# Optimization experiments

Hardware: AMD Instinct MI355X
Metric: run time of the kernel (lower is better)

Reference implementation:

```python
import jax, jax.numpy as jnp
import numpy as np

D_MODEL = 768
N_HEADS = 12
D_K = D_MODEL // N_HEADS
BATCH = 1
SEQ = 4096


def setup_inputs() -> dict:
    key = jax.random.key(0)
    kx, kq, kk, kv, ko = jax.random.split(key, 5)
    s = 1.0 / np.sqrt(D_MODEL)
    return {
        "x": jax.random.normal(kx, (BATCH, SEQ, D_MODEL), dtype=jnp.float32),
        "wq": jax.random.normal(kq, (D_MODEL, D_MODEL), dtype=jnp.float32) * s,
        "wk": jax.random.normal(kk, (D_MODEL, D_MODEL), dtype=jnp.float32) * s,
        "wv": jax.random.normal(kv, (D_MODEL, D_MODEL), dtype=jnp.float32) * s,
        "wo": jax.random.normal(ko, (D_MODEL, D_MODEL), dtype=jnp.float32) * s,
    }


def reference(x, wq, wk, wv, wo):
    B, S, D = x.shape
    H, dk = N_HEADS, D_K
    # nn.Linear(x) = x @ W.T ; reshape to [B,H,S,dk]
    def proj(w):
        return (x @ w.T).reshape(B, S, H, dk).transpose(0, 2, 1, 3)
    q, k, v = proj(wq), proj(wk), proj(wv)
    scores = jnp.einsum('bhqd,bhkd->bhqk', q, k) / np.sqrt(dk).astype(np.float32)
    attn = jax.nn.softmax(scores, axis=-1)
    out = jnp.einsum('bhqk,bhkd->bhqd', attn, v)
    out = out.transpose(0, 2, 1, 3).reshape(B, S, D)
    return out @ wo.T
```

## Files before the change

kernel.cpp:

```cpp
#include <hip/hip_runtime.h>
#include <stdint.h>

#define SEQ 4096
#define DMODEL 768
#define NHEADS 12
#define DKH 64

typedef __attribute__((ext_vector_type(8))) short short8;
typedef __attribute__((ext_vector_type(4))) float floatx4;
typedef __attribute__((ext_vector_type(16))) float floatx16;

__device__ __forceinline__ unsigned short f2bf(float f) {
    unsigned int u = __float_as_uint(f);
    u += 0x7fffu + ((u >> 16) & 1u);
    return (unsigned short)(u >> 16);
}

__device__ __forceinline__ float exp2fast(float x) {
    return __builtin_amdgcn_exp2f(x);
}

__device__ __forceinline__ unsigned int cvt_pk_bf16(float lo, float hi) {
    unsigned int r;
    asm("v_cvt_pk_bf16_f32 %0, %1, %2" : "=v"(r) : "v"(lo), "v"(hi));
    return r;
}

__device__ __forceinline__ int swz(int row, int colb) {
    return colb ^ ((row & 7) << 4);
}

__device__ __forceinline__ void async_copy16(void* lds, const void* g) {
    __builtin_amdgcn_global_load_lds(
        (const __attribute__((address_space(1))) void*)g,
        (__attribute__((address_space(3))) void*)lds,
        16, 0, 0);
}

__global__ __launch_bounds__(256) void castk(const float* __restrict__ src,
                                             unsigned short* __restrict__ dst,
                                             int n4) {
    int i = blockIdx.x * 256 + threadIdx.x;
    if (i >= n4) return;
    float4 v = ((const float4*)src)[i];
    ushort4 o;
    o.x = f2bf(v.x); o.y = f2bf(v.y); o.z = f2bf(v.z); o.w = f2bf(v.w);
    ((ushort4*)dst)[i] = o;
}

__global__ __launch_bounds__(256) void castw(const float* __restrict__ w0,
                                             const float* __restrict__ w1,
                                             const float* __restrict__ w2,
                                             const float* __restrict__ w3,
                                             unsigned short* __restrict__ dst) {
    int b = blockIdx.x;
    int wsel = b / 576;
    int i = (b % 576) * 256 + threadIdx.x;
    const float* src = (wsel == 0) ? w0 : (wsel == 1) ? w1 : (wsel == 2) ? w2 : w3;
    float4 v = ((const float4*)src)[i];
    ushort4 o;
    o.x = f2bf(v.x); o.y = f2bf(v.y); o.z = f2bf(v.z); o.w = f2bf(v.w);
    ((ushort4*)(dst + (size_t)wsel * 589824))[i] = o;
}

#define STAGE_G(bsel, kb)                                                              \
    do {                                                                               \
        char* As_ = smem + (bsel) * 24576;                                             \
        _Pragma("unroll") for (int ii = 0; ii < 4; ii++) {                             \
            int o = ii * 4096 + t * 16;                                                \
            int row = o >> 7, colb = o & 127;                                          \
            async_copy16(As_ + ii * 4096 + wid * 1024,                                 \
                         (const char*)A + ((size_t)(rowBase + row) * DMODEL + (kb)) * 2 \
                             + swz(row, colb));                                        \
        }                                                                              \
        _Pragma("unroll") for (int ii = 0; ii < 2; ii++) {                             \
            int o = ii * 4096 + t * 16;                                                \
            int row = o >> 7, colb = o & 127;                                          \
            async_copy16(As_ + 16384 + ii * 4096 + wid * 1024,                         \
                         (const char*)B + ((size_t)(colBase + row) * DMODEL + (kb)) * 2 \
                             + swz(row, colb));                                        \
        }                                                                              \
    } while (0)

#define GEMM_COMPUTE(As, Bs)                                                           \
    do {                                                                               \
        short8 a_[4][2], b_[2][2];                                                     \
        _Pragma("unroll") for (int m = 0; m < 4; m++)                                  \
            _Pragma("unroll") for (int kk = 0; kk < 2; kk++) {                         \
                int row = wr * 64 + m * 16 + lr;                                       \
                int colb = kk * 64 + lg * 16;                                          \
                a_[m][kk] = *(const short8*)((As) + row * 128 + swz(row, colb));       \
            }                                                                          \
        _Pragma("unroll") for (int n = 0; n < 2; n++)                                  \
            _Pragma("unroll") for (int kk = 0; kk < 2; kk++) {                         \
                int row = wc * 32 + n * 16 + lr;                                       \
                int colb = kk * 64 + lg * 16;                                          \
                b_[n][kk] = *(const short8*)((Bs) + row * 128 + swz(row, colb));       \
            }                                                                          \
        _Pragma("unroll") for (int m = 0; m < 4; m++)                                  \
            _Pragma("unroll") for (int n = 0; n < 2; n++)                              \
                _Pragma("unroll") for (int kk = 0; kk < 2; kk++)                       \
                    acc[m][n] = __builtin_amdgcn_mfma_f32_16x16x32_bf16(               \
                        a_[m][kk], b_[n][kk], acc[m][n], 0, 0, 0);                     \
    } while (0)

__global__ __launch_bounds__(256, 2)
void gemm_qkv(const unsigned short* __restrict__ A,
              const unsigned short* __restrict__ W,
              unsigned short* __restrict__ OutBase, float qscale) {
    __shared__ __align__(128) char smem[49152];

    const int t = threadIdx.x;
    const int wid = t >> 6, lane = t & 63;
    const int lr = lane & 15, lg = lane >> 4;
    const int wr = wid >> 1, wc = wid & 1;
    const int rowBase = blockIdx.x * 128;
    const int proj = blockIdx.y / 12;
    const int colBase = (blockIdx.y % 12) * 64;
    const unsigned short* B = W + (size_t)proj * 589824;

    const floatx4 zero4 = {0.f, 0.f, 0.f, 0.f};
    floatx4 acc[4][2];
#pragma unroll
    for (int m = 0; m < 4; m++)
#pragma unroll
        for (int n = 0; n < 2; n++) acc[m][n] = zero4;

    STAGE_G(0, 0);
    for (int i = 0; i < 12; ++i) {
        __builtin_amdgcn_s_barrier();
        __builtin_amdgcn_sched_barrier(0);
        if (i < 11) {
            STAGE_G((i + 1) & 1, (i + 1) * 64);
            asm volatile("s_waitcnt vmcnt(6)" ::: "memory");
        } else {
            asm volatile("s_waitcnt vmcnt(0)" ::: "memory");
        }
        __builtin_amdgcn_s_barrier();
        __builtin_amdgcn_sched_barrier(0);
        char* As = smem + (i & 1) * 24576;
        GEMM_COMPUTE(As, As + 16384);
    }

    if (proj < 2) {
        unsigned short* O = OutBase + (size_t)proj * 3145728;
        float scale = (proj == 0) ? qscale : 1.0f;
#pragma unroll
        for (int m = 0; m < 4; m++)
#pragma unroll
            for (int n = 0; n < 2; n++)
#pragma unroll
                for (int r = 0; r < 4; r++) {
                    int srow = rowBase + wr * 64 + m * 16 + lg * 4 + r;
                    int col = colBase + wc * 32 + n * 16 + lr;
                    int h = col >> 6, d = col & 63;
                    O[((size_t)h * SEQ + srow) * DKH + d] = f2bf(acc[m][n][r] * scale);
                }
    } else {
        unsigned short* O = OutBase + 6291456;
#pragma unroll
        for (int m = 0; m < 4; m++)
#pragma unroll
            for (int n = 0; n < 2; n++) {
                int srow0 = rowBase + wr * 64 + m * 16 + lg * 4;
                int pos0 = (srow0 & ~15) | ((srow0 & 4) << 1) | ((srow0 & 8) >> 1);
                int col = colBase + wc * 32 + n * 16 + lr;
                ushort4 o4;
                o4.x = f2bf(acc[m][n][0]);
                o4.y = f2bf(acc[m][n][1]);
                o4.z = f2bf(acc[m][n][2]);
                o4.w = f2bf(acc[m][n][3]);
                *(ushort4*)(O + (size_t)col * SEQ + pos0) = o4;
            }
    }
}

__global__ __launch_bounds__(256, 2)
void gemm_o(const unsigned short* __restrict__ A,
            const unsigned short* __restrict__ B,
            float* __restrict__ Out) {
    __shared__ __align__(128) char smem[49152];

    const int t = threadIdx.x;
    const int wid = t >> 6, lane = t & 63;
    const int lr = lane & 15, lg = lane >> 4;
    const int wr = wid >> 1, wc = wid & 1;
    const int rowBase = blockIdx.x * 128;
    const int colBase = blockIdx.y * 64;

    const floatx4 zero4 = {0.f, 0.f, 0.f, 0.f};
    floatx4 acc[4][2];
#pragma unroll
    for (int m = 0; m < 4; m++)
#pragma unroll
        for (int n = 0; n < 2; n++) acc[m][n] = zero4;

    STAGE_G(0, 0);
    for (int i = 0; i < 12; ++i) {
        __builtin_amdgcn_s_barrier();
        __builtin_amdgcn_sched_barrier(0);
        if (i < 11) {
            STAGE_G((i + 1) & 1, (i + 1) * 64);
            asm volatile("s_waitcnt vmcnt(6)" ::: "memory");
        } else {
            asm volatile("s_waitcnt vmcnt(0)" ::: "memory");
        }
        __builtin_amdgcn_s_barrier();
        __builtin_amdgcn_sched_barrier(0);
        char* As = smem + (i & 1) * 24576;
        GEMM_COMPUTE(As, As + 16384);
    }

#pragma unroll
    for (int m = 0; m < 4; m++)
#pragma unroll
        for (int n = 0; n < 2; n++)
#pragma unroll
            for (int r = 0; r < 4; r++) {
                int srow = rowBase + wr * 64 + m * 16 + lg * 4 + r;
                int col = colBase + wc * 32 + n * 16 + lr;
                Out[(size_t)srow * DMODEL + col] = acc[m][n][r];
            }
}

#define STAGE_KA(bsel, kv0)                                                            \
    do {                                                                               \
        char* Kd_ = smem + (bsel) * 16384;                                             \
        _Pragma("unroll") for (int ii = 0; ii < 8; ii++) {                             \
            int o = ii * 2048 + t * 16;                                                \
            int row = o >> 7, colb = o & 127;                                          \
            async_copy16(Kd_ + ii * 2048 + wid * 1024,                                 \
                         (const char*)(Kp + headOff + (size_t)((kv0) + row) * DKH)     \
                             + swz(row, colb));                                        \
        }                                                                              \
    } while (0)

#define STAGE_VA(kv0)                                                                  \
    do {                                                                               \
        char* Vd_ = smem + 32768;                                                      \
        _Pragma("unroll") for (int hh = 0; hh < 2; hh++)                               \
            _Pragma("unroll") for (int ii = 0; ii < 4; ii++) {                         \
                int o = ii * 2048 + t * 16;                                            \
                int row = o >> 7, colb = o & 127;                                      \
                async_copy16(Vd_ + hh * 8192 + ii * 2048 + wid * 1024,                 \
                             (const char*)(Vt + (size_t)(h * DKH + row) * SEQ          \
                                           + (kv0) + hh * 64) + swz(row, colb));       \
            }                                                                          \
    } while (0)

__global__ __launch_bounds__(128, 2)
void attn_k(const unsigned short* __restrict__ Q,
            const unsigned short* __restrict__ Kp,
            const unsigned short* __restrict__ Vt,
            unsigned short* __restrict__ AO) {
    __shared__ __align__(128) char smem[49152];

    const int t = threadIdx.x;
    const int wid = t >> 6, lane = t & 63;
    const int q31 = lane & 31, hi = lane >> 5;

    int nid = (blockIdx.x & 7) * 96 + (blockIdx.x >> 3);
    const int h = nid >> 6, qb = nid & 63;
    const size_t headOff = (size_t)h * SEQ * DKH;

    const unsigned short* qptr =
        Q + headOff + (size_t)(qb * 64 + wid * 32 + q31) * DKH + hi * 8;
    short8 qf[4];
#pragma unroll
    for (int ks = 0; ks < 4; ks++) qf[ks] = *(const short8*)(qptr + ks * 16);

    const floatx16 z16 = {0.f, 0.f, 0.f, 0.f, 0.f, 0.f, 0.f, 0.f,
                          0.f, 0.f, 0.f, 0.f, 0.f, 0.f, 0.f, 0.f};
    float mrun = -3.0e38f, lrun = 0.f;
    floatx16 accO[2] = {z16, z16};

    STAGE_KA(0, 0);

    for (int tt = 0; tt < 32; ++tt) {
        asm volatile("s_waitcnt vmcnt(0)" ::: "memory");
        __builtin_amdgcn_s_barrier();
        __builtin_amdgcn_sched_barrier(0);
        STAGE_VA(tt * 128);
        if (tt < 31) STAGE_KA((tt + 1) & 1, (tt + 1) * 128);
        __builtin_amdgcn_sched_barrier(0);

        const char* Ks = smem + (tt & 1) * 16384;
        const char* Vs = smem + 32768;

        floatx16 s[4] = {z16, z16, z16, z16};
        __builtin_amdgcn_s_setprio(1);
#pragma unroll
        for (int kb = 0; kb < 4; kb++)
#pragma unroll
            for (int ks = 0; ks < 4; ks++) {
                int row = kb * 32 + q31;
                int byteo = (row * 128 + ks * 32 + hi * 16) ^ ((q31 & 7) << 4);
                short8 kf = *(const short8*)(Ks + byteo);
                s[kb] = __builtin_amdgcn_mfma_f32_32x32x16_bf16(kf, qf[ks], s[kb], 0, 0, 0);
            }
        __builtin_amdgcn_s_setprio(0);

        float mk[4];
#pragma unroll
        for (int kb = 0; kb < 4; kb++) {
            float a = fmaxf(fmaxf(s[kb][0], s[kb][1]), fmaxf(s[kb][2], s[kb][3]));
            float b = fmaxf(fmaxf(s[kb][4], s[kb][5]), fmaxf(s[kb][6], s[kb][7]));
            float c = fmaxf(fmaxf(s[kb][8], s[kb][9]), fmaxf(s[kb][10], s[kb][11]));
            float d = fmaxf(fmaxf(s[kb][12], s[kb][13]), fmaxf(s[kb][14], s[kb][15]));
            mk[kb] = fmaxf(fmaxf(a, b), fmaxf(c, d));
        }
        float mt = fmaxf(fmaxf(mk[0], mk[1]), fmaxf(mk[2], mk[3]));
        mt = fmaxf(mt, __shfl_xor(mt, 32));
        if (!__all(mt <= mrun + 8.0f)) {
            float mnew = fmaxf(mrun, mt);
            float al = exp2fast(mrun - mnew);
#pragma unroll
            for (int fb = 0; fb < 2; fb++)
#pragma unroll
                for (int j = 0; j < 16; j++) accO[fb][j] *= al;
            lrun *= al;
            mrun = mnew;
        }
#pragma unroll
        for (int kb = 0; kb < 4; kb++)
#pragma unroll
            for (int j = 0; j < 16; j++) s[kb][j] = exp2fast(s[kb][j] - mrun);
        float sum = 0.f;
#pragma unroll
        for (int kb = 0; kb < 4; kb++) {
            float a = (s[kb][0] + s[kb][1]) + (s[kb][2] + s[kb][3]);
            float b = (s[kb][4] + s[kb][5]) + (s[kb][6] + s[kb][7]);
            float c = (s[kb][8] + s[kb][9]) + (s[kb][10] + s[kb][11]);
            float d = (s[kb][12] + s[kb][13]) + (s[kb][14] + s[kb][15]);
            sum += (a + b) + (c + d);
        }
        sum += __shfl_xor(sum, 32);
        lrun += sum;

        if (tt < 31) asm volatile("s_waitcnt vmcnt(8)" ::: "memory");
        else         asm volatile("s_waitcnt vmcnt(0)" ::: "memory");
        __builtin_amdgcn_s_barrier();
        __builtin_amdgcn_sched_barrier(0);

        __builtin_amdgcn_s_setprio(1);
#pragma unroll
        for (int c = 0; c < 8; c++) {
            const int kb = c >> 1, r0 = (c & 1) * 8;
            uint4 pw;
            pw.x = cvt_pk_bf16(s[kb][r0 + 0], s[kb][r0 + 1]);
            pw.y = cvt_pk_bf16(s[kb][r0 + 2], s[kb][r0 + 3]);
            pw.z = cvt_pk_bf16(s[kb][r0 + 4], s[kb][r0 + 5]);
            pw.w = cvt_pk_bf16(s[kb][r0 + 6], s[kb][r0 + 7]);
            short8 pf = *(const short8*)&pw;
#pragma unroll
            for (int fb = 0; fb < 2; fb++) {
                int row = fb * 32 + q31;
                int byteo = ((c >> 2) * 8192 + row * 128 + (c & 3) * 32 + hi * 16)
                            ^ ((q31 & 7) << 4);
                short8 vf = *(const short8*)(Vs + byteo);
                accO[fb] = __builtin_amdgcn_mfma_f32_32x32x16_bf16(vf, pf, accO[fb], 0, 0, 0);
            }
        }
        __builtin_amdgcn_s_setprio(0);
    }

    float inv = 1.0f / lrun;
    int srow = qb * 64 + wid * 32 + q31;
#pragma unroll
    for (int fb = 0; fb < 2; fb++)
#pragma unroll
        for (int rq = 0; rq < 4; rq++) {
            ushort4 o4;
            o4.x = f2bf(accO[fb][4 * rq + 0] * inv);
            o4.y = f2bf(accO[fb][4 * rq + 1] * inv);
            o4.z = f2bf(accO[fb][4 * rq + 2] * inv);
            o4.w = f2bf(accO[fb][4 * rq + 3] * inv);
            int col = h * DKH + fb * 32 + rq * 8 + hi * 4;
            *(ushort4*)(AO + (size_t)srow * DMODEL + col) = o4;
        }
}

extern "C" void kernel_launch(void* const* d_in, const int* in_sizes, int n_in,
                              void* d_out, int out_size, void* d_ws, size_t ws_size,
                              hipStream_t stream) {
    const float* x  = (const float*)d_in[0];
    const float* wq = (const float*)d_in[1];
    const float* wk = (const float*)d_in[2];
    const float* wv = (const float*)d_in[3];
    const float* wo = (const float*)d_in[4];

    char* ws = (char*)d_ws;
    unsigned short* xb  = (unsigned short*)(ws + 0);
    unsigned short* wqb = (unsigned short*)(ws + 6291456);
    unsigned short* wob = (unsigned short*)(ws + 9830400);
    unsigned short* Qb  = (unsigned short*)(ws + 11010048);
    unsigned short* Kb  = (unsigned short*)(ws + 17301504);
    unsigned short* VTb = (unsigned short*)(ws + 23592960);
    unsigned short* AOb = (unsigned short*)(ws + 29884416);

    castk<<<3072, 256, 0, stream>>>(x, xb, 786432);
    castw<<<2304, 256, 0, stream>>>(wq, wk, wv, wo, wqb);

    gemm_qkv<<<dim3(32, 36), 256, 0, stream>>>(xb, wqb, Qb, 0.18033688f);

    attn_k<<<dim3(768), 128, 0, stream>>>(Qb, Kb, VTb, AOb);

    gemm_o<<<dim3(32, 12), 256, 0, stream>>>(AOb, wob, (float*)d_out);
}
```

Measured before the change: 131.4 us.

## Split attention KV tile across wave pairs and merge partial softmax states

The attention kernel goes from 128 to 256 threads per block. Each pair of waves shares one 32-query group, and each wave in the pair handles half of every 128-key tile, so per-wave MFMA and softmax work per tile is halved. At the end the two waves combine their running max, sum and accumulators through shared memory. K and V staging is relaid out into an MFMA-fragment-ordered, swizzle-free LDS layout so each lane reads contiguous 16-byte chunks. This adds threads, a final merge step and a different launch-bounds occupancy target, and risks LDS bank conflicts from the new layout.

```diff
diff --git a/kernel.cpp b/kernel.cpp
--- a/kernel.cpp
+++ b/kernel.cpp
@@ -223,32 +223,36 @@
             }
 }
 
-#define STAGE_KA(bsel, kv0)                                                            \
+#define STAGE_K8(bsel, kv0)                                                            \
     do {                                                                               \
         char* Kd_ = smem + (bsel) * 16384;                                             \
-        _Pragma("unroll") for (int ii = 0; ii < 8; ii++) {                             \
-            int o = ii * 2048 + t * 16;                                                \
-            int row = o >> 7, colb = o & 127;                                          \
-            async_copy16(Kd_ + ii * 2048 + wid * 1024,                                 \
-                         (const char*)(Kp + headOff + (size_t)((kv0) + row) * DKH)     \
-                             + swz(row, colb));                                        \
+        _Pragma("unroll") for (int ii = 0; ii < 4; ii++) {                             \
+            int cc = ii * 256 + wid * 64 + lane;                                       \
+            int gk = cc >> 6, qd = (cc >> 1) & 31, hh = cc & 1;                        \
+            int kb2 = gk >> 2, ks2 = gk & 3;                                           \
+            int key = kb2 * 32 + qd;                                                   \
+            async_copy16(Kd_ + (ii * 256 + wid * 64) * 16,                             \
+                         (const char*)(Kp + headOff) + (size_t)((kv0) + key) * 128     \
+                             + (ks2 * 2 + hh) * 16);                                   \
         }                                                                              \
     } while (0)
 
-#define STAGE_VA(kv0)                                                                  \
+#define STAGE_V8(kv0)                                                                  \
     do {                                                                               \
         char* Vd_ = smem + 32768;                                                      \
-        _Pragma("unroll") for (int hh = 0; hh < 2; hh++)                               \
-            _Pragma("unroll") for (int ii = 0; ii < 4; ii++) {                         \
-                int o = ii * 2048 + t * 16;                                            \
-                int row = o >> 7, colb = o & 127;                                      \
-                async_copy16(Vd_ + hh * 8192 + ii * 2048 + wid * 1024,                 \
-                             (const char*)(Vt + (size_t)(h * DKH + row) * SEQ          \
-                                           + (kv0) + hh * 64) + swz(row, colb));       \
-            }                                                                          \
+        _Pragma("unroll") for (int ii = 0; ii < 4; ii++) {                             \
+            int cc = ii * 256 + wid * 64 + lane;                                       \
+            int gv = cc >> 6, qd = (cc >> 1) & 31, hh = cc & 1;                        \
+            int fbv = gv & 1, cv = (gv >> 1) & 3, ev = gv >> 3;                        \
+            int feat = fbv * 32 + qd;                                                  \
+            int p0 = ev * 64 + cv * 16 + hh * 8;                                       \
+            async_copy16(Vd_ + (ii * 256 + wid * 64) * 16,                             \
+                         (const char*)Vt                                               \
+                             + ((size_t)(h * DKH + feat) * SEQ + (kv0) + p0) * 2);     \
+        }                                                                              \
     } while (0)
 
-__global__ __launch_bounds__(128, 2)
+__global__ __launch_bounds__(256, 3)
 void attn_k(const unsigned short* __restrict__ Q,
             const unsigned short* __restrict__ Kp,
             const unsigned short* __restrict__ Vt,
@@ -258,13 +262,14 @@
     const int t = threadIdx.x;
     const int wid = t >> 6, lane = t & 63;
     const int q31 = lane & 31, hi = lane >> 5;
+    const int g = wid >> 1, e = wid & 1;
 
     int nid = (blockIdx.x & 7) * 96 + (blockIdx.x >> 3);
     const int h = nid >> 6, qb = nid & 63;
     const size_t headOff = (size_t)h * SEQ * DKH;
 
     const unsigned short* qptr =
-        Q + headOff + (size_t)(qb * 64 + wid * 32 + q31) * DKH + hi * 8;
+        Q + headOff + (size_t)(qb * 64 + g * 32 + q31) * DKH + hi * 8;
     short8 qf[4];
 #pragma unroll
     for (int ks = 0; ks < 4; ks++) qf[ks] = *(const short8*)(qptr + ks * 16);
@@ -274,42 +279,43 @@
     float mrun = -3.0e38f, lrun = 0.f;
     floatx16 accO[2] = {z16, z16};
 
-    STAGE_KA(0, 0);
+    STAGE_K8(0, 0);
 
     for (int tt = 0; tt < 32; ++tt) {
         asm volatile("s_waitcnt vmcnt(0)" ::: "memory");
         __builtin_amdgcn_s_barrier();
         __builtin_amdgcn_sched_barrier(0);
-        STAGE_VA(tt * 128);
-        if (tt < 31) STAGE_KA((tt + 1) & 1, (tt + 1) * 128);
+        STAGE_V8(tt * 128);
+        if (tt < 31) STAGE_K8((tt + 1) & 1, (tt + 1) * 128);
         __builtin_amdgcn_sched_barrier(0);
 
         const char* Ks = smem + (tt & 1) * 16384;
         const char* Vs = smem + 32768;
 
-        floatx16 s[4] = {z16, z16, z16, z16};
+        floatx16 s[2] = {z16, z16};
         __builtin_amdgcn_s_setprio(1);
 #pragma unroll
-        for (int kb = 0; kb < 4; kb++)
+        for (int kb = 0; kb < 2; kb++) {
+            const int kb2 = e * 2 + kb;
 #pragma unroll
             for (int ks = 0; ks < 4; ks++) {
-                int row = kb * 32 + q31;
-                int byteo = (row * 128 + ks * 32 + hi * 16) ^ ((q31 & 7) << 4);
-                short8 kf = *(const short8*)(Ks + byteo);
+                short8 kf = *(const short8*)(
+                    Ks + ((kb2 * 4 + ks) * 64 + q31 * 2 + hi) * 16);
                 s[kb] = __builtin_amdgcn_mfma_f32_32x32x16_bf16(kf, qf[ks], s[kb], 0, 0, 0);
             }
+        }
         __builtin_amdgcn_s_setprio(0);
 
-        float mk[4];
-#pragma unroll
-        for (int kb = 0; kb < 4; kb++) {
+        float mk[2];
+#pragma unroll
+        for (int kb = 0; kb < 2; kb++) {
             float a = fmaxf(fmaxf(s[kb][0], s[kb][1]), fmaxf(s[kb][2], s[kb][3]));
             float b = fmaxf(fmaxf(s[kb][4], s[kb][5]), fmaxf(s[kb][6], s[kb][7]));
             float c = fmaxf(fmaxf(s[kb][8], s[kb][9]), fmaxf(s[kb][10], s[kb][11]));
             float d = fmaxf(fmaxf(s[kb][12], s[kb][13]), fmaxf(s[kb][14], s[kb][15]));
             mk[kb] = fmaxf(fmaxf(a, b), fmaxf(c, d));
         }
-        float mt = fmaxf(fmaxf(mk[0], mk[1]), fmaxf(mk[2], mk[3]));
+        float mt = fmaxf(mk[0], mk[1]);
         mt = fmaxf(mt, __shfl_xor(mt, 32));
         if (!__all(mt <= mrun + 8.0f)) {
             float mnew = fmaxf(mrun, mt);
@@ -322,12 +328,12 @@
             mrun = mnew;
         }
 #pragma unroll
-        for (int kb = 0; kb < 4; kb++)
+        for (int kb = 0; kb < 2; kb++)
 #pragma unroll
             for (int j = 0; j < 16; j++) s[kb][j] = exp2fast(s[kb][j] - mrun);
         float sum = 0.f;
 #pragma unroll
-        for (int kb = 0; kb < 4; kb++) {
+        for (int kb = 0; kb < 2; kb++) {
             float a = (s[kb][0] + s[kb][1]) + (s[kb][2] + s[kb][3]);
             float b = (s[kb][4] + s[kb][5]) + (s[kb][6] + s[kb][7]);
             float c = (s[kb][8] + s[kb][9]) + (s[kb][10] + s[kb][11]);
@@ -337,14 +343,14 @@
         sum += __shfl_xor(sum, 32);
         lrun += sum;
 
-        if (tt < 31) asm volatile("s_waitcnt vmcnt(8)" ::: "memory");
+        if (tt < 31) asm volatile("s_waitcnt vmcnt(4)" ::: "memory");
         else         asm volatile("s_waitcnt vmcnt(0)" ::: "memory");
         __builtin_amdgcn_s_barrier();
         __builtin_amdgcn_sched_barrier(0);
 
         __builtin_amdgcn_s_setprio(1);
 #pragma unroll
-        for (int c = 0; c < 8; c++) {
+        for (int c = 0; c < 4; c++) {
             const int kb = c >> 1, r0 = (c & 1) * 8;
             uint4 pw;
             pw.x = cvt_pk_bf16(s[kb][r0 + 0], s[kb][r0 + 1]);
@@ -354,30 +360,52 @@
             short8 pf = *(const short8*)&pw;
 #pragma unroll
             for (int fb = 0; fb < 2; fb++) {
-                int row = fb * 32 + q31;
-                int byteo = ((c >> 2) * 8192 + row * 128 + (c & 3) * 32 + hi * 16)
-                            ^ ((q31 & 7) << 4);
-                short8 vf = *(const short8*)(Vs + byteo);
+                short8 vf = *(const short8*)(
+                    Vs + (((e * 4 + c) * 2 + fb) * 64 + q31 * 2 + hi) * 16);
                 accO[fb] = __builtin_amdgcn_mfma_f32_32x32x16_bf16(vf, pf, accO[fb], 0, 0, 0);
             }
         }
         __builtin_amdgcn_s_setprio(0);
     }
 
-    float inv = 1.0f / lrun;
-    int srow = qb * 64 + wid * 32 + q31;
-#pragma unroll
-    for (int fb = 0; fb < 2; fb++)
-#pragma unroll
-        for (int rq = 0; rq < 4; rq++) {
-            ushort4 o4;
-            o4.x = f2bf(accO[fb][4 * rq + 0] * inv);
-            o4.y = f2bf(accO[fb][4 * rq + 1] * inv);
-            o4.z = f2bf(accO[fb][4 * rq + 2] * inv);
-            o4.w = f2bf(accO[fb][4 * rq + 3] * inv);
-            int col = h * DKH + fb * 32 + rq * 8 + hi * 4;
-            *(ushort4*)(AO + (size_t)srow * DMODEL + col) = o4;
-        }
+    __builtin_amdgcn_s_barrier();
+    char* R = smem + g * 9216 + lane * 144;
+    if (e == 1) {
+#pragma unroll
+        for (int fb = 0; fb < 2; fb++)
+#pragma unroll
+            for (int j4 = 0; j4 < 4; j4++) {
+                floatx4 v4 = {accO[fb][j4 * 4 + 0], accO[fb][j4 * 4 + 1],
+                              accO[fb][j4 * 4 + 2], accO[fb][j4 * 4 + 3]};
+                *(floatx4*)(R + fb * 64 + j4 * 16) = v4;
+            }
+        *(float*)(R + 128) = mrun;
+        *(float*)(R + 132) = lrun;
+        asm volatile("s_waitcnt lgkmcnt(0)" ::: "memory");
+    }
+    __builtin_amdgcn_s_barrier();
+    __builtin_amdgcn_sched_barrier(0);
+    if (e == 0) {
+        float m1 = *(const float*)(R + 128);
+        float l1 = *(const float*)(R + 132);
+        float m = fmaxf(mrun, m1);
+        float a0 = exp2fast(mrun - m), a1 = exp2fast(m1 - m);
+        float inv = 1.0f / (lrun * a0 + l1 * a1);
+        int srow = qb * 64 + g * 32 + q31;
+#pragma unroll
+        for (int fb = 0; fb < 2; fb++)
+#pragma unroll
+            for (int rq = 0; rq < 4; rq++) {
+                floatx4 p4 = *(const floatx4*)(R + fb * 64 + rq * 16);
+                ushort4 o4;
+                o4.x = f2bf((accO[fb][4 * rq + 0] * a0 + p4[0] * a1) * inv);
+                o4.y = f2bf((accO[fb][4 * rq + 1] * a0 + p4[1] * a1) * inv);
+                o4.z = f2bf((accO[fb][4 * rq + 2] * a0 + p4[2] * a1) * inv);
+                o4.w = f2bf((accO[fb][4 * rq + 3] * a0 + p4[3] * a1) * inv);
+                int col = h * DKH + fb * 32 + rq * 8 + hi * 4;
+                *(ushort4*)(AO + (size_t)srow * DMODEL + col) = o4;
+            }
+    }
 }
 
 extern "C" void kernel_launch(void* const* d_in, const int* in_sizes, int n_in,
@@ -403,7 +431,7 @@
 
     gemm_qkv<<<dim3(32, 36), 256, 0, stream>>>(xb, wqb, Qb, 0.18033688f);
 
-    attn_k<<<dim3(768), 128, 0, stream>>>(Qb, Kb, VTb, AOb);
+    attn_k<<<dim3(768), 256, 0, stream>>>(Qb, Kb, VTb, AOb);
 
     gemm_o<<<dim3(32, 12), 256, 0, stream>>>(AOb, wob, (float*)d_out);
 }
```

After: 119.5 us (median of 3 runs). -9.0%, faster.
